# Kernel optimization log

Hardware: AMD Instinct MI355X
Metric: run time of the kernel (lower is better)

## Reference

```python
import jax, jax.numpy as jnp
import numpy as np

B, C_IN, C_OUT, K, H, W = 8, 64, 64, 3, 128, 128
CTX = max(8, C_OUT // 4)  # 16


def setup_inputs() -> dict:
    key = jax.random.key(0)
    ks = jax.random.split(key, 6)
    x = jax.random.normal(ks[0], (B, C_IN, H, W), dtype=jnp.float32)
    # context_proj: 1x1 conv (ctx_ch, C_in) + bias
    ctx_w = jax.random.normal(ks[1], (CTX, C_IN), dtype=jnp.float32) * (1.0 / np.sqrt(C_IN))
    ctx_b = jnp.zeros((CTX,), dtype=jnp.float32)
    # kernel_gen: Linear(ctx_ch -> C_out*C_in*K*K), init std=0.001, zero bias
    kg_w = jax.random.normal(ks[2], (C_OUT * C_IN * K * K, CTX), dtype=jnp.float32) * 0.001
    kg_b = jnp.zeros((C_OUT * C_IN * K * K,), dtype=jnp.float32)
    gamma = jnp.zeros((C_OUT,), dtype=jnp.float32)
    bias = jnp.zeros((C_OUT,), dtype=jnp.float32)
    # value_proj: 1x1 conv (C_in, C_in), no bias
    value_w = jax.random.normal(ks[3], (C_IN, C_IN), dtype=jnp.float32) * (1.0 / np.sqrt(C_IN))
    return {"x": x, "ctx_w": ctx_w, "ctx_b": ctx_b, "kg_w": kg_w, "kg_b": kg_b,
            "gamma": gamma, "bias": bias, "value_w": value_w}


def reference(x, ctx_w, ctx_b, kg_w, kg_b, gamma, bias, value_w):
    b = x.shape[0]
    # context projection (1x1 conv) + global average pool -> (B, CTX)
    ctx = jnp.einsum('bchw,oc->bohw', x, ctx_w) + ctx_b[None, :, None, None]
    ctx_vec = jnp.mean(ctx, axis=(2, 3))  # (B, CTX)
    # per-sample kernel generation
    kernels_flat = ctx_vec @ kg_w.T + kg_b  # (B, O*C*K*K)
    kernels = jnp.tanh(kernels_flat.reshape(b, C_OUT, C_IN, K, K))
    mean_k = jnp.mean(kernels.reshape(b, C_OUT, -1), axis=-1)  # (B, O)
    lam = jax.nn.sigmoid(gamma)[None, :, None, None, None]
    kernels = kernels - lam * mean_k[:, :, None, None, None]
    # value projection (1x1 conv, no bias)
    v = jnp.einsum('bchw,oc->bohw', x, value_w)
    # unfold: patches (B, C*K*K, H, W), feature order (C, kh, kw) matching F.unfold
    pad = K // 2
    patches = jax.lax.conv_general_dilated_patches(
        v, filter_shape=(K, K), window_strides=(1, 1),
        padding=[(pad, pad), (pad, pad)])  # (B, C*K*K, H, W)
    out = jnp.einsum('bof,bfhw->bohw', kernels.reshape(b, C_OUT, -1), patches)
    out = out + bias[None, :, None, None]
    return jax.nn.relu(out)
```

## Files before the change

### kernel.cpp

```cpp
#include <hip/hip_runtime.h>
#include <stdint.h>

#define NB 8
#define CIN 64
#define COUT 64
#define HH 128
#define WW 128

typedef unsigned short ushort_t;
typedef unsigned int uint_t;
typedef __attribute__((ext_vector_type(8))) __bf16 bf16x8;
typedef __attribute__((ext_vector_type(4))) float f32x4;

__device__ __forceinline__ ushort_t f2bf(float f) {
  uint_t u = __builtin_bit_cast(uint_t, f);
  u += 0x7fffu + ((u >> 16) & 1u);
  return (ushort_t)(u >> 16);
}

#define WS_XSUM 0
#define WS_XT   2048
#define WS_A    16779264

__global__ void k_zero(float* p) {
  int i = blockIdx.x * 256 + threadIdx.x;
  if (i < 512) p[i] = 0.f;
}

__global__ void k_trans(const float* __restrict__ x, ushort_t* __restrict__ xT,
                        float* __restrict__ xsum) {
  __shared__ float tile[64 * 129];
  int b = blockIdx.x >> 7;
  int h = blockIdx.x & 127;
  int tid = threadIdx.x;
  int w = tid & 127;
  int ch = tid >> 7;
  const float* xp = x + ((size_t)(b * 64) * 128 + h) * 128 + w;
#pragma unroll
  for (int p = 0; p < 32; ++p) {
    int c = p * 2 + ch;
    tile[c * 129 + w] = xp[(size_t)c * 16384];
  }
  __syncthreads();
  if (tid < 64) {
    float s = 0.f;
#pragma unroll 8
    for (int w2 = 0; w2 < 128; ++w2) s += tile[tid * 129 + w2];
    atomicAdd(&xsum[b * 64 + tid], s);
  }
#pragma unroll
  for (int it = 0; it < 4; ++it) {
    int chunk = tid + it * 256;
    int w2 = chunk >> 3;
    int cc = chunk & 7;
    union { ushort_t u[8]; int4 v; } pk;
#pragma unroll
    for (int j = 0; j < 8; ++j) pk.u[j] = f2bf(tile[(cc * 8 + j) * 129 + w2]);
    *reinterpret_cast<int4*>(xT + (((size_t)(b * 128 + h) * 128 + w2) * 64 + cc * 8)) = pk.v;
  }
}

__global__ void k_gen(const float* __restrict__ xsum,
                      const float* __restrict__ ctx_w, const float* __restrict__ ctx_b,
                      const float* __restrict__ kg_w, const float* __restrict__ kg_b,
                      const float* __restrict__ gamma, const float* __restrict__ value_w,
                      ushort_t* __restrict__ A) {
  __shared__ float xm[64];
  __shared__ float ctxv[16];
  __shared__ float ks_[576];
  __shared__ float red[256];
  __shared__ float vw[4096];
  int b = blockIdx.x >> 6;
  int o = blockIdx.x & 63;
  int tid = threadIdx.x;
  if (tid < 64) xm[tid] = xsum[b * 64 + tid] * (1.f / 16384.f);
#pragma unroll
  for (int p = 0; p < 16; ++p) vw[tid + p * 256] = value_w[tid + p * 256];
  __syncthreads();
  if (tid < 16) {
    float s = ctx_b[tid];
#pragma unroll 8
    for (int c = 0; c < 64; ++c) s += xm[c] * ctx_w[tid * 64 + c];
    ctxv[tid] = s;
  }
  __syncthreads();
  float val[3] = {0.f, 0.f, 0.f};
  float partial = 0.f;
#pragma unroll
  for (int p = 0; p < 3; ++p) {
    int i = tid + p * 256;
    if (i < 576) {
      int n = o * 576 + i;
      float s = kg_b[n];
      const float* kwp = kg_w + (size_t)n * 16;
#pragma unroll
      for (int j = 0; j < 16; ++j) s += ctxv[j] * kwp[j];
      val[p] = tanhf(s);
      partial += val[p];
    }
  }
  red[tid] = partial;
  __syncthreads();
  for (int s = 128; s > 0; s >>= 1) {
    if (tid < s) red[tid] += red[tid + s];
    __syncthreads();
  }
  float mean = red[0] * (1.f / 576.f);
  float lam = 1.f / (1.f + expf(-gamma[o]));
#pragma unroll
  for (int p = 0; p < 3; ++p) {
    int i = tid + p * 256;
    if (i < 576) ks_[i] = val[p] - lam * mean;
  }
  __syncthreads();
  ushort_t* Ao = A + (size_t)(b * 64 + o) * 576;
#pragma unroll
  for (int p = 0; p < 3; ++p) {
    int f = tid + p * 256;
    if (f < 576) {
      int tap = f >> 6;
      int c = f & 63;
      float s = 0.f;
#pragma unroll 8
      for (int cp = 0; cp < 64; ++cp) s += ks_[cp * 9 + tap] * vw[cp * 64 + c];
      Ao[f] = f2bf(s);
    }
  }
}

__launch_bounds__(256)
__global__ void k_conv(const ushort_t* __restrict__ xT, const ushort_t* __restrict__ A,
                       const float* __restrict__ bias, float* __restrict__ out) {
  __shared__ __align__(16) ushort_t xs[6 * 34 * 72];
  int bx = blockIdx.x;
  int b = bx >> 7;
  int rem = bx & 127;
  int h0 = (rem >> 2) * 4;
  int w0 = (rem & 3) * 32;
  int tid = threadIdx.x;
  int wave = tid >> 6;
  int lane = tid & 63;
  int n16 = lane & 15;
  int q = lane >> 4;

  bf16x8 af[18];
  const ushort_t* Ag = A + (size_t)(b * 64 + wave * 16 + n16) * 576 + q * 8;
#pragma unroll
  for (int ks = 0; ks < 18; ++ks)
    af[ks] = *reinterpret_cast<const bf16x8*>(Ag + ks * 32);

  const ushort_t* xb = xT + (size_t)b * 128 * 128 * 64;
#pragma unroll
  for (int it = 0; it < 7; ++it) {
    int chunk = tid + it * 256;
    if (chunk < 1632) {
      int lr = chunk / 272;
      int r2 = chunk - lr * 272;
      int lc = r2 >> 3;
      int cc = r2 & 7;
      int hh = h0 - 1 + lr;
      int ww = w0 - 1 + lc;
      int4 v = make_int4(0, 0, 0, 0);
      if (hh >= 0 && hh < 128 && ww >= 0 && ww < 128)
        v = *reinterpret_cast<const int4*>(xb + ((size_t)(hh * 128 + ww) * 64 + cc * 8));
      *reinterpret_cast<int4*>(xs + ((lr * 34 + lc) * 72 + cc * 8)) = v;
    }
  }
  __syncthreads();

  f32x4 acc[8];
#pragma unroll
  for (int i = 0; i < 8; ++i) acc[i] = (f32x4){0.f, 0.f, 0.f, 0.f};

  const ushort_t* xsl = xs + n16 * 72 + q * 8;
#pragma unroll
  for (int rr = 0; rr < 4; ++rr) {
#pragma unroll
    for (int cb = 0; cb < 2; ++cb) {
      int nt = rr * 2 + cb;
#pragma unroll
      for (int tap = 0; tap < 9; ++tap) {
        int kh = tap / 3, kw2 = tap % 3;
#pragma unroll
        for (int cq = 0; cq < 2; ++cq) {
          bf16x8 bf = *reinterpret_cast<const bf16x8*>(
              xsl + ((rr + kh) * 34 + cb * 16 + kw2) * 72 + cq * 32);
          acc[nt] = __builtin_amdgcn_mfma_f32_16x16x32_bf16(af[tap * 2 + cq], bf, acc[nt], 0, 0, 0);
        }
      }
    }
  }

#pragma unroll
  for (int rr = 0; rr < 4; ++rr) {
#pragma unroll
    for (int cb = 0; cb < 2; ++cb) {
      int nt = rr * 2 + cb;
      int hcur = h0 + rr;
      int wcur = w0 + cb * 16 + n16;
#pragma unroll
      for (int r = 0; r < 4; ++r) {
        int o = wave * 16 + q * 4 + r;
        float v = acc[nt][r] + bias[o];
        v = fmaxf(v, 0.f);
        out[((size_t)(b * 64 + o) * 128 + hcur) * 128 + wcur] = v;
      }
    }
  }
}

extern "C" void kernel_launch(void* const* d_in, const int* in_sizes, int n_in,
                              void* d_out, int out_size, void* d_ws, size_t ws_size,
                              hipStream_t stream) {
  const float* x       = (const float*)d_in[0];
  const float* ctx_w   = (const float*)d_in[1];
  const float* ctx_b   = (const float*)d_in[2];
  const float* kg_w    = (const float*)d_in[3];
  const float* kg_b    = (const float*)d_in[4];
  const float* gamma   = (const float*)d_in[5];
  const float* bias    = (const float*)d_in[6];
  const float* value_w = (const float*)d_in[7];
  float* out = (float*)d_out;

  float* xsum  = (float*)((char*)d_ws + WS_XSUM);
  ushort_t* xT = (ushort_t*)((char*)d_ws + WS_XT);
  ushort_t* A  = (ushort_t*)((char*)d_ws + WS_A);

  k_zero<<<2, 256, 0, stream>>>(xsum);
  k_trans<<<1024, 256, 0, stream>>>(x, xT, xsum);
  k_gen<<<512, 256, 0, stream>>>(xsum, ctx_w, ctx_b, kg_w, kg_b, gamma, value_w, A);
  k_conv<<<1024, 256, 0, stream>>>(xT, A, bias, out);
}
```

Baseline: 126.3 us.

## Double conv row tile and reuse each LDS fragment across kernel rows

The conv kernel now processes 8 output rows per block instead of 4, halving the grid and reducing the halo overhead of the staged input tile. The inner loop is reorganised so each bf16 input fragment loaded from LDS feeds up to three MFMAs, one per kernel row, which cuts LDS reads. Accumulators double to 16 per thread and launch bounds now request 2 blocks per SM, which raises register pressure. The transpose kernel's per-channel row sum is also split across all 256 threads with a small shared-memory reduction instead of running serially on 64 threads.

Result: no change. 125.7 us (-0.5%).

```diff
diff --git a/kernel.cpp b/kernel.cpp
--- a/kernel.cpp
+++ b/kernel.cpp
@@ -30,6 +30,7 @@
 __global__ void k_trans(const float* __restrict__ x, ushort_t* __restrict__ xT,
                         float* __restrict__ xsum) {
   __shared__ float tile[64 * 129];
+  __shared__ float red[256];
   int b = blockIdx.x >> 7;
   int h = blockIdx.x & 127;
   int tid = threadIdx.x;
@@ -42,10 +43,17 @@
     tile[c * 129 + w] = xp[(size_t)c * 16384];
   }
   __syncthreads();
+  {
+    int c = tid >> 2;
+    int w4 = (tid & 3) * 32;
+    float s = 0.f;
+#pragma unroll
+    for (int w2 = 0; w2 < 32; ++w2) s += tile[c * 129 + w4 + w2];
+    red[tid] = s;
+  }
+  __syncthreads();
   if (tid < 64) {
-    float s = 0.f;
-#pragma unroll 8
-    for (int w2 = 0; w2 < 128; ++w2) s += tile[tid * 129 + w2];
+    float s = red[tid * 4] + red[tid * 4 + 1] + red[tid * 4 + 2] + red[tid * 4 + 3];
     atomicAdd(&xsum[b * 64 + tid], s);
   }
 #pragma unroll
@@ -128,14 +136,14 @@
   }
 }
 
-__launch_bounds__(256)
+__launch_bounds__(256, 2)
 __global__ void k_conv(const ushort_t* __restrict__ xT, const ushort_t* __restrict__ A,
                        const float* __restrict__ bias, float* __restrict__ out) {
-  __shared__ __align__(16) ushort_t xs[6 * 34 * 72];
+  __shared__ __align__(16) ushort_t xs[10 * 34 * 72];
   int bx = blockIdx.x;
-  int b = bx >> 7;
-  int rem = bx & 127;
-  int h0 = (rem >> 2) * 4;
+  int b = bx >> 6;
+  int rem = bx & 63;
+  int h0 = (rem >> 2) * 8;
   int w0 = (rem & 3) * 32;
   int tid = threadIdx.x;
   int wave = tid >> 6;
@@ -151,9 +159,9 @@
 
   const ushort_t* xb = xT + (size_t)b * 128 * 128 * 64;
 #pragma unroll
-  for (int it = 0; it < 7; ++it) {
+  for (int it = 0; it < 11; ++it) {
     int chunk = tid + it * 256;
-    if (chunk < 1632) {
+    if (chunk < 2720) {
       int lr = chunk / 272;
       int r2 = chunk - lr * 272;
       int lc = r2 >> 3;
@@ -168,31 +176,36 @@
   }
   __syncthreads();
 
-  f32x4 acc[8];
-#pragma unroll
-  for (int i = 0; i < 8; ++i) acc[i] = (f32x4){0.f, 0.f, 0.f, 0.f};
+  f32x4 acc[16];
+#pragma unroll
+  for (int i = 0; i < 16; ++i) acc[i] = (f32x4){0.f, 0.f, 0.f, 0.f};
 
   const ushort_t* xsl = xs + n16 * 72 + q * 8;
 #pragma unroll
-  for (int rr = 0; rr < 4; ++rr) {
+  for (int ar = 0; ar < 10; ++ar) {
 #pragma unroll
     for (int cb = 0; cb < 2; ++cb) {
-      int nt = rr * 2 + cb;
-#pragma unroll
-      for (int tap = 0; tap < 9; ++tap) {
-        int kh = tap / 3, kw2 = tap % 3;
+#pragma unroll
+      for (int kw2 = 0; kw2 < 3; ++kw2) {
 #pragma unroll
         for (int cq = 0; cq < 2; ++cq) {
           bf16x8 bf = *reinterpret_cast<const bf16x8*>(
-              xsl + ((rr + kh) * 34 + cb * 16 + kw2) * 72 + cq * 32);
-          acc[nt] = __builtin_amdgcn_mfma_f32_16x16x32_bf16(af[tap * 2 + cq], bf, acc[nt], 0, 0, 0);
+              xsl + (ar * 34 + cb * 16 + kw2) * 72 + cq * 32);
+#pragma unroll
+          for (int kh = 0; kh < 3; ++kh) {
+            int rr = ar - kh;
+            if (rr >= 0 && rr < 8) {
+              acc[rr * 2 + cb] = __builtin_amdgcn_mfma_f32_16x16x32_bf16(
+                  af[(kh * 3 + kw2) * 2 + cq], bf, acc[rr * 2 + cb], 0, 0, 0);
+            }
+          }
         }
       }
     }
   }
 
 #pragma unroll
-  for (int rr = 0; rr < 4; ++rr) {
+  for (int rr = 0; rr < 8; ++rr) {
 #pragma unroll
     for (int cb = 0; cb < 2; ++cb) {
       int nt = rr * 2 + cb;
@@ -229,5 +242,5 @@
   k_zero<<<2, 256, 0, stream>>>(xsum);
   k_trans<<<1024, 256, 0, stream>>>(x, xT, xsum);
   k_gen<<<512, 256, 0, stream>>>(xsum, ctx_w, ctx_b, kg_w, kg_b, gamma, value_w, A);
-  k_conv<<<1024, 256, 0, stream>>>(xT, A, bias, out);
-}
+  k_conv<<<512, 256, 0, stream>>>(xT, A, bias, out);
+}
```
